# Optimization experiments

Measured on AMD Instinct MI355X. Metric: run time of the kernel, lower is better.

## Reference

```python
import jax, jax.numpy as jnp
import numpy as np
from jax import lax

STRIDE = 2
PADDING = 2
EPS = 1e-5


def _conv1d(x, w):
    # x: (N, C_in, T), w: (C_out, C_in, K) -> (N, C_out, T_out)
    return lax.conv_general_dilated(
        x, w, window_strides=(STRIDE,), padding=[(PADDING, PADDING)],
        dimension_numbers=("NCH", "OIH", "NCH"))


def setup_inputs() -> dict:
    key = jax.random.key(0)
    ks = jax.random.split(key, 5)
    Batch, num_sensors, in_c, out_c, k, T, r = 32, 8, 64, 128, 5, 2048, 8
    x = jax.random.normal(ks[0], (Batch * num_sensors, in_c, T), dtype=jnp.float32)
    A_flat = jax.random.normal(ks[1], (Batch, r * in_c * k), dtype=jnp.float32) * 0.02
    B_flat = jax.random.normal(ks[2], (Batch, out_c * r), dtype=jnp.float32) * 0.02
    fan_in = in_c * k
    conv_w = jax.random.normal(ks[3], (out_c, in_c, k), dtype=jnp.float32) / np.sqrt(fan_in)
    conv_b = jax.random.normal(ks[4], (out_c,), dtype=jnp.float32) * 0.01
    gamma = jnp.ones((out_c,), dtype=jnp.float32)
    beta = jnp.zeros((out_c,), dtype=jnp.float32)
    return {"x": x, "A_flat": A_flat, "B_flat": B_flat,
            "conv_w": conv_w, "conv_b": conv_b, "gamma": gamma, "beta": beta,
            "num_sensors": num_sensors, "r": r, "lora_scale": 0.5}


def reference(x, A_flat, B_flat, conv_w, conv_b, gamma, beta, num_sensors, r, lora_scale):
    Batch = A_flat.shape[0]
    out_c, in_c, k = conv_w.shape
    T = x.shape[-1]

    # base conv1d
    out_base = _conv1d(x, conv_w) + conv_b[None, :, None]  # (B*S, out_c, T_out)

    # dynamic per-sample LoRA delta weight: delta_W = B @ A, (Batch, out_c, in_c, k)
    A = A_flat.reshape(Batch, r, in_c * k)
    B_mat = B_flat.reshape(Batch, out_c, r)
    delta_W = jnp.einsum("bor,brm->bom", B_mat, A).reshape(Batch, out_c, in_c, k)
    delta_W = delta_W * lora_scale

    # per-sample conv: sensors of one sample share that sample's delta weight
    x_b = x.reshape(Batch, num_sensors, in_c, T)
    lora_out = jax.vmap(_conv1d)(x_b, delta_W)  # (Batch, S, out_c, T_out)
    lora_out = lora_out.reshape(Batch * num_sensors, out_c, -1)

    out = jax.nn.relu(out_base + lora_out)

    # GroupNorm, num_groups = min(4, out_c) reduced until divisible
    G = min(4, out_c)
    while out_c % G != 0:
        G -= 1
    N, C, To = out.shape
    og = out.reshape(N, G, C // G, To)
    mean = og.mean(axis=(2, 3), keepdims=True)
    var = og.var(axis=(2, 3), keepdims=True)
    normed = ((og - mean) * lax.rsqrt(var + EPS)).reshape(N, C, To)
    return normed * gamma[None, :, None] + beta[None, :, None]
```

## Files before the change

kernel.cpp:

```cpp
#include <hip/hip_runtime.h>
#include <hip/hip_bf16.h>

#define EPSV 1e-5f
#define PITCH 36
#define NCOL 2052

typedef short bf16x8 __attribute__((ext_vector_type(8)));
typedef short bf16x4 __attribute__((ext_vector_type(4)));
typedef float f32x4  __attribute__((ext_vector_type(4)));

__device__ __forceinline__ short f2bf(float f){
  unsigned u = __float_as_uint(f);
  u += 0x7fff + ((u >> 16) & 1);
  return (short)(u >> 16);
}
__device__ __forceinline__ int pk2(float a, float b){
  __hip_bfloat162 h = __float22bfloat162_rn(float2{a, b});
  return *reinterpret_cast<int*>(&h);
}

__device__ __forceinline__ int swz(int col, int slot){
  return col * PITCH + 4 * (slot ^ ((col >> 4) & 3));
}

__global__ void build_weights(const float* __restrict__ A_flat,
                              const float* __restrict__ B_flat,
                              const float* __restrict__ conv_w,
                              const float* __restrict__ scale_p,
                              short* __restrict__ Wb){
  int idx = blockIdx.x * 256 + threadIdx.x;
  int ci = idx & 63;
  int co = (idx >> 6) & 127;
  int bj = idx >> 13;
  int b  = bj / 5;
  int j  = bj - 5 * b;
  int m  = ci * 5 + j;
  const float* Bp = B_flat + (b * 128 + co) * 8;
  const float* Ap = A_flat + b * 8 * 320 + m;
  float d = 0.f;
#pragma unroll
  for (int r = 0; r < 8; ++r) d = fmaf(Bp[r], Ap[r * 320], d);
  float w = conv_w[co * 320 + m] + scale_p[0] * d;
  Wb[idx] = f2bf(w);
}

__global__ __launch_bounds__(512, 2)
void conv_gn_mfma(const float* __restrict__ x,
                  const short* __restrict__ Wb,
                  const float* __restrict__ conv_b,
                  const float* __restrict__ gamma,
                  const float* __restrict__ beta,
                  float* __restrict__ out){
  __shared__ short xl[NCOL * PITCH];
  __shared__ float redS[8], redQ[8], bc2[2];

  const int bid    = blockIdx.x;
  const int sample = ((bid & 7) << 5) + (bid >> 5);
  const int g      = (bid >> 3) & 3;
  const int b      = sample >> 3;
  const int tid    = threadIdx.x;
  const int lane   = tid & 63;
  const int wid    = tid >> 6;
  const int l16    = lane & 15;
  const int lk     = lane >> 4;
  const int t0w    = wid << 7;

  f32x4 acc[2][8];
#pragma unroll
  for (int m2 = 0; m2 < 2; ++m2)
#pragma unroll
    for (int n = 0; n < 8; ++n) acc[m2][n] = (f32x4){0.f, 0.f, 0.f, 0.f};

  const size_t wb_base = (size_t)b * 5 * 128 * 64;

  for (int ch = 0; ch < 2; ++ch) {
    if (ch) __syncthreads();
    {
      const float* xs = x + ((size_t)sample * 64 + ch * 32 + wid * 4) * 2048;
      if (tid < 72) {
        int cc = tid / 18, dw = tid % 18;
        int col = (cc < 2) ? cc : (2048 + cc);
        *(int*)((char*)xl + col * 72 + dw * 4) = 0;
      }
#pragma unroll 2
      for (int pass = 0; pass < 8; ++pass) {
        int cb = pass * 256 + lane * 4;
        const float4 v0 = *(const float4*)(xs + 0 * 2048 + cb);
        const float4 v1 = *(const float4*)(xs + 1 * 2048 + cb);
        const float4 v2 = *(const float4*)(xs + 2 * 2048 + cb);
        const float4 v3 = *(const float4*)(xs + 3 * 2048 + cb);
        bf16x4 p0 = {f2bf(v0.x), f2bf(v1.x), f2bf(v2.x), f2bf(v3.x)};
        bf16x4 p1 = {f2bf(v0.y), f2bf(v1.y), f2bf(v2.y), f2bf(v3.y)};
        bf16x4 p2 = {f2bf(v0.z), f2bf(v1.z), f2bf(v2.z), f2bf(v3.z)};
        bf16x4 p3 = {f2bf(v0.w), f2bf(v1.w), f2bf(v2.w), f2bf(v3.w)};
        const int c0 = cb + 2;
        *(bf16x4*)&xl[swz(c0,     wid)] = p0;
        *(bf16x4*)&xl[swz(c0 + 1, wid)] = p1;
        *(bf16x4*)&xl[swz(c0 + 2, wid)] = p2;
        *(bf16x4*)&xl[swz(c0 + 3, wid)] = p3;
      }
    }
    __syncthreads();
#pragma unroll
    for (int j = 0; j < 5; ++j) {
      const short* apb = Wb + wb_base + ((size_t)j * 128 + g * 32) * 64 + ch * 32 + lk * 8;
      bf16x8 a0 = *(const bf16x8*)(apb + (size_t)(l16)      * 64);
      bf16x8 a1 = *(const bf16x8*)(apb + (size_t)(l16 + 16) * 64);
#pragma unroll
      for (int n = 0; n < 8; ++n) {
        int c = 2 * (t0w + n * 16 + l16) + j;
        bf16x4 lo = *(const bf16x4*)&xl[swz(c, 2 * lk)];
        bf16x4 hi = *(const bf16x4*)&xl[swz(c, 2 * lk + 1)];
        bf16x8 bfr = {lo[0], lo[1], lo[2], lo[3], hi[0], hi[1], hi[2], hi[3]};
        acc[0][n] = __builtin_amdgcn_mfma_f32_16x16x32_bf16(a0, bfr, acc[0][n], 0, 0, 0);
        acc[1][n] = __builtin_amdgcn_mfma_f32_16x16x32_bf16(a1, bfr, acc[1][n], 0, 0, 0);
      }
    }
  }

  float cb_[2][4], ga_[2][4], be_[2][4];
#pragma unroll
  for (int m2 = 0; m2 < 2; ++m2)
#pragma unroll
    for (int r = 0; r < 4; ++r) {
      int co = g * 32 + m2 * 16 + lk * 4 + r;
      cb_[m2][r] = conv_b[co];
      ga_[m2][r] = gamma[co];
      be_[m2][r] = beta[co];
    }
  float s1 = 0.f, s2 = 0.f;
#pragma unroll
  for (int m2 = 0; m2 < 2; ++m2)
#pragma unroll
    for (int n = 0; n < 8; ++n)
#pragma unroll
      for (int r = 0; r < 4; ++r) {
        float v = acc[m2][n][r] + cb_[m2][r];
        v = v > 0.f ? v : 0.f;
        acc[m2][n][r] = v;
        s1 += v;
        s2 = fmaf(v, v, s2);
      }
#pragma unroll
  for (int off = 32; off; off >>= 1) {
    s1 += __shfl_down(s1, off);
    s2 += __shfl_down(s2, off);
  }
  if (lane == 0) { redS[wid] = s1; redQ[wid] = s2; }
  __syncthreads();
  if (tid == 0) {
    float a = 0.f, q = 0.f;
#pragma unroll
    for (int w = 0; w < 8; ++w) { a += redS[w]; q += redQ[w]; }
    float mean = a * (1.f / 32768.f);
    float var  = q * (1.f / 32768.f) - mean * mean;
    bc2[0] = mean;
    bc2[1] = rsqrtf(var + EPSV);
  }
  __syncthreads();
  const float mean = bc2[0], inv = bc2[1];
  float* ob = out + (size_t)sample * 128 * 1024;
#pragma unroll
  for (int m2 = 0; m2 < 2; ++m2)
#pragma unroll
    for (int r = 0; r < 4; ++r) {
      int co = g * 32 + m2 * 16 + lk * 4 + r;
      float aa = ga_[m2][r] * inv;
      float bb = be_[m2][r] - mean * aa;
      float* orow = ob + (size_t)co * 1024 + t0w + l16;
#pragma unroll
      for (int n = 0; n < 8; ++n)
        orow[n * 16] = acc[m2][n][r] * aa + bb;
    }
}

extern "C" void kernel_launch(void* const* d_in, const int* in_sizes, int n_in,
                              void* d_out, int out_size, void* d_ws, size_t ws_size,
                              hipStream_t stream) {
  const float* x       = (const float*)d_in[0];
  const float* A_flat  = (const float*)d_in[1];
  const float* B_flat  = (const float*)d_in[2];
  const float* conv_w  = (const float*)d_in[3];
  const float* conv_b  = (const float*)d_in[4];
  const float* gamma   = (const float*)d_in[5];
  const float* beta    = (const float*)d_in[6];
  const float* scale_p = (const float*)d_in[9];

  float* out = (float*)d_out;
  short* Wb  = (short*)d_ws;

  build_weights<<<5120, 256, 0, stream>>>(A_flat, B_flat, conv_w, scale_p, Wb);
  conv_gn_mfma<<<1024, 512, 0, stream>>>(x, Wb, conv_b, gamma, beta, out);
}
```

Baseline: 92.08 us.

## Process two GroupNorm groups per block to reuse staged input tile

```diff
diff --git a/kernel.cpp b/kernel.cpp
--- a/kernel.cpp
+++ b/kernel.cpp
@@ -13,10 +13,6 @@
   unsigned u = __float_as_uint(f);
   u += 0x7fff + ((u >> 16) & 1);
   return (short)(u >> 16);
-}
-__device__ __forceinline__ int pk2(float a, float b){
-  __hip_bfloat162 h = __float22bfloat162_rn(float2{a, b});
-  return *reinterpret_cast<int*>(&h);
 }
 
 __device__ __forceinline__ int swz(int col, int slot){
@@ -52,26 +48,29 @@
                   const float* __restrict__ beta,
                   float* __restrict__ out){
   __shared__ short xl[NCOL * PITCH];
-  __shared__ float redS[8], redQ[8], bc2[2];
+  __shared__ float redS[8], redQ[8], bcv[2][2];
 
   const int bid    = blockIdx.x;
-  const int sample = ((bid & 7) << 5) + (bid >> 5);
-  const int g      = (bid >> 3) & 3;
+  const int sample = ((bid & 7) << 5) + (bid >> 4);
+  const int h      = (bid >> 3) & 1;
   const int b      = sample >> 3;
   const int tid    = threadIdx.x;
   const int lane   = tid & 63;
   const int wid    = tid >> 6;
   const int l16    = lane & 15;
   const int lk     = lane >> 4;
-  const int t0w    = wid << 7;
+  const int q      = wid & 1;
+  const int tq     = wid >> 1;
+  const int t0w    = tq << 8;
 
-  f32x4 acc[2][8];
+  f32x4 acc[2][16];
 #pragma unroll
   for (int m2 = 0; m2 < 2; ++m2)
 #pragma unroll
-    for (int n = 0; n < 8; ++n) acc[m2][n] = (f32x4){0.f, 0.f, 0.f, 0.f};
+    for (int n = 0; n < 16; ++n) acc[m2][n] = (f32x4){0.f, 0.f, 0.f, 0.f};
 
   const size_t wb_base = (size_t)b * 5 * 128 * 64;
+  const int cobase = h * 64 + q * 32;
 
   for (int ch = 0; ch < 2; ++ch) {
     if (ch) __syncthreads();
@@ -103,11 +102,11 @@
     __syncthreads();
 #pragma unroll
     for (int j = 0; j < 5; ++j) {
-      const short* apb = Wb + wb_base + ((size_t)j * 128 + g * 32) * 64 + ch * 32 + lk * 8;
+      const short* apb = Wb + wb_base + ((size_t)j * 128 + cobase) * 64 + ch * 32 + lk * 8;
       bf16x8 a0 = *(const bf16x8*)(apb + (size_t)(l16)      * 64);
       bf16x8 a1 = *(const bf16x8*)(apb + (size_t)(l16 + 16) * 64);
 #pragma unroll
-      for (int n = 0; n < 8; ++n) {
+      for (int n = 0; n < 16; ++n) {
         int c = 2 * (t0w + n * 16 + l16) + j;
         bf16x4 lo = *(const bf16x4*)&xl[swz(c, 2 * lk)];
         bf16x4 hi = *(const bf16x4*)&xl[swz(c, 2 * lk + 1)];
@@ -123,7 +122,7 @@
   for (int m2 = 0; m2 < 2; ++m2)
 #pragma unroll
     for (int r = 0; r < 4; ++r) {
-      int co = g * 32 + m2 * 16 + lk * 4 + r;
+      int co = cobase + m2 * 16 + lk * 4 + r;
       cb_[m2][r] = conv_b[co];
       ga_[m2][r] = gamma[co];
       be_[m2][r] = beta[co];
@@ -132,7 +131,7 @@
 #pragma unroll
   for (int m2 = 0; m2 < 2; ++m2)
 #pragma unroll
-    for (int n = 0; n < 8; ++n)
+    for (int n = 0; n < 16; ++n)
 #pragma unroll
       for (int r = 0; r < 4; ++r) {
         float v = acc[m2][n][r] + cb_[m2][r];
@@ -148,28 +147,28 @@
   }
   if (lane == 0) { redS[wid] = s1; redQ[wid] = s2; }
   __syncthreads();
-  if (tid == 0) {
-    float a = 0.f, q = 0.f;
+  if (tid < 2) {
+    float a = 0.f, qq = 0.f;
 #pragma unroll
-    for (int w = 0; w < 8; ++w) { a += redS[w]; q += redQ[w]; }
+    for (int w = 0; w < 4; ++w) { a += redS[tid + 2 * w]; qq += redQ[tid + 2 * w]; }
     float mean = a * (1.f / 32768.f);
-    float var  = q * (1.f / 32768.f) - mean * mean;
-    bc2[0] = mean;
-    bc2[1] = rsqrtf(var + EPSV);
+    float var  = qq * (1.f / 32768.f) - mean * mean;
+    bcv[tid][0] = mean;
+    bcv[tid][1] = rsqrtf(var + EPSV);
   }
   __syncthreads();
-  const float mean = bc2[0], inv = bc2[1];
+  const float mean = bcv[q][0], inv = bcv[q][1];
   float* ob = out + (size_t)sample * 128 * 1024;
 #pragma unroll
   for (int m2 = 0; m2 < 2; ++m2)
 #pragma unroll
     for (int r = 0; r < 4; ++r) {
-      int co = g * 32 + m2 * 16 + lk * 4 + r;
+      int co = cobase + m2 * 16 + lk * 4 + r;
       float aa = ga_[m2][r] * inv;
       float bb = be_[m2][r] - mean * aa;
       float* orow = ob + (size_t)co * 1024 + t0w + l16;
 #pragma unroll
-      for (int n = 0; n < 8; ++n)
+      for (int n = 0; n < 16; ++n)
         orow[n * 16] = acc[m2][n][r] * aa + bb;
     }
 }
@@ -190,5 +189,5 @@
   short* Wb  = (short*)d_ws;
 
   build_weights<<<5120, 256, 0, stream>>>(A_flat, B_flat, conv_w, scale_p, Wb);
-  conv_gn_mfma<<<1024, 512, 0, stream>>>(x, Wb, conv_b, gamma, beta, out);
+  conv_gn_mfma<<<512, 512, 0, stream>>>(x, Wb, conv_b, gamma, beta, out);
 }
```

Result: slower. 162.5 us (+76.5%).
